# Kernel optimization log

Hardware: AMD Instinct MI355X
Metric: run time of the kernel (lower is better)

Reference implementation:

```python
import jax, jax.numpy as jnp
import numpy as np

M = 2          # interp_dim
D = 4          # interp_degree
MESH_LOWER = np.array([0.0, 0.0], dtype=np.float32)
MESH_UPPER = np.array([1.0, 1.0], dtype=np.float32)
MESH_SIZE = np.array([64, 64], dtype=np.int32)   # coe grid = mesh_size*D+1 = [257, 257]


def _lagrange_basis(t):
    """t: [N, M] local coordinate in [0, D]; returns bases [N, M, D+1].
    L_j(t) = prod_{k != j} (t - k) / (j - k)."""
    ks = jnp.arange(D + 1, dtype=t.dtype)
    tk = t[..., None] - ks                       # [N, M, D+1]
    bs = []
    for j in range(D + 1):                       # small fixed loop over D+1=5 bases
        num = jnp.ones(t.shape, t.dtype)
        denom = 1.0
        for k in range(D + 1):
            if k != j:
                num = num * tk[..., k]
                denom *= float(j - k)
        bs.append(num / denom)
    return jnp.stack(bs, axis=-1)                # [N, M, D+1]


def setup_inputs() -> dict:
    key = jax.random.key(0)
    k1, k2 = jax.random.split(key)
    inputs = jax.random.uniform(k1, (2048, 2048, M), dtype=jnp.float32)  # points in [0,1)^2
    grid = tuple(int(s) * D + 1 for s in MESH_SIZE)                      # (257, 257)
    interp_coe = jax.random.normal(k2, grid, dtype=jnp.float32)
    return {"inputs": inputs, "interp_coe": interp_coe}


def reference(inputs, interp_coe):
    size = inputs.shape
    x = inputs.reshape(-1, M)                                   # [N, M]
    lower = jnp.asarray(MESH_LOWER, x.dtype)
    upper = jnp.asarray(MESH_UPPER, x.dtype)
    msize = jnp.asarray(MESH_SIZE.astype(np.float32), x.dtype)
    u = (x - lower) / (upper - lower) * msize                   # grid coordinates
    cell = jnp.clip(jnp.floor(u), 0.0, msize - 1.0)             # [N, M] element index
    t = (u - cell) * D                                          # local coord in [0, D]
    basis = _lagrange_basis(t)                                  # [N, M, D+1]
    base = cell.astype(jnp.int32) * D                           # [N, M] global node base index
    offs = jnp.arange(D + 1, dtype=jnp.int32)
    i0 = base[:, 0, None] + offs                                # [N, D+1]
    i1 = base[:, 1, None] + offs                                # [N, D+1]
    coe = interp_coe[i0[:, :, None], i1[:, None, :]]            # [N, D+1, D+1] gathered cell coes
    out = jnp.einsum('nij,ni,nj->n', coe, basis[:, 0], basis[:, 1])
    return out.reshape(size[:-1])
```

## Files before the change

kernel.cpp:

```cpp
#include <hip/hip_runtime.h>

#define NGRID 257
#define LDS_PITCH 260
#define LDS_BYTES (LDS_PITCH * NGRID * 2)
#define BLOCK 1024
#define GRID 256
#define ITERS 16

typedef _Float16 half2_t __attribute__((ext_vector_type(2)));
typedef _Float16 half4_t __attribute__((ext_vector_type(4)));

struct __attribute__((packed, aligned(4))) f4u { float x, y, z, w; };

__device__ __forceinline__ half2_t pack2(float a, float b) {
    return __builtin_bit_cast(half2_t, __builtin_amdgcn_cvt_pkrtz(a, b));
}

__device__ __forceinline__ void lag_basis(float t, float b[5]) {
    float f0 = t;
    float f1 = t - 1.0f;
    float f2 = t - 2.0f;
    float f3 = t - 3.0f;
    float f4 = t - 4.0f;
    float p01 = f0 * f1;
    float p12 = f1 * f2;
    float p23 = f2 * f3;
    float p34 = f3 * f4;
    b[0] = p12 * p34 * (1.0f / 24.0f);
    b[1] = f0 * f2 * p34 * (-1.0f / 6.0f);
    b[2] = p01 * p34 * (1.0f / 4.0f);
    b[3] = p01 * f2 * f4 * (-1.0f / 6.0f);
    b[4] = p01 * p23 * (1.0f / 24.0f);
}

__device__ __forceinline__ float eval_pt(const _Float16* __restrict__ lds,
                                         float x0, float x1) {
    float u0 = x0 * 64.0f, u1 = x1 * 64.0f;
    int ic0 = (int)u0;
    int ic1 = (int)u1;
    float t0 = __builtin_amdgcn_fractf(u0) * 4.0f;
    float t1 = __builtin_amdgcn_fractf(u1) * 4.0f;

    const _Float16* base  = lds + (ic0 * 4) * LDS_PITCH + ic1 * 4;
    const _Float16* base2 = base + 2 * LDS_PITCH;

    half4_t lo0 = *(const half4_t*)(base);
    half4_t lo1 = *(const half4_t*)(base + LDS_PITCH);
    half4_t lo2 = *(const half4_t*)(base2);
    half4_t lo3 = *(const half4_t*)(base2 + LDS_PITCH);
    half4_t lo4 = *(const half4_t*)(base2 + 2 * LDS_PITCH);
    half2_t h0 = *(const half2_t*)(base + 4);
    half2_t h1 = *(const half2_t*)(base + LDS_PITCH + 4);
    half2_t h2 = *(const half2_t*)(base2 + 4);
    half2_t h3 = *(const half2_t*)(base2 + LDS_PITCH + 4);
    half2_t h4 = *(const half2_t*)(base2 + 2 * LDS_PITCH + 4);

    float b0[5], b1[5];
    lag_basis(t0, b0);
    lag_basis(t1, b1);
    half2_t b01 = pack2(b1[0], b1[1]);
    half2_t b23 = pack2(b1[2], b1[3]);

    half4_t lo[5] = { lo0, lo1, lo2, lo3, lo4 };
    half2_t hi[5] = { h0, h1, h2, h3, h4 };
    float rd[5];
#pragma unroll
    for (int i = 0; i < 5; ++i) {
        half2_t xy = __builtin_shufflevector(lo[i], lo[i], 0, 1);
        half2_t zw = __builtin_shufflevector(lo[i], lo[i], 2, 3);
        float r = (float)hi[i][0] * b1[4];
        r = __builtin_amdgcn_fdot2(zw, b23, r, false);
        r = __builtin_amdgcn_fdot2(xy, b01, r, false);
        rd[i] = r;
    }
    float accA = b0[4] * rd[4];
    accA = fmaf(b0[0], rd[0], accA);
    accA = fmaf(b0[2], rd[2], accA);
    float accB = b0[1] * rd[1];
    accB = fmaf(b0[3], rd[3], accB);
    return accA + accB;
}

__launch_bounds__(BLOCK, 4)
__global__ void lagrange_kernel(const float* __restrict__ inputs,
                                const float* __restrict__ coe,
                                float* __restrict__ out,
                                int npts) {
    extern __shared__ _Float16 lds[];
    const int t = threadIdx.x;

#pragma unroll
    for (int k = 0; k < 16; ++k) {
        int g = t + k * BLOCK;
        int r = g >> 6;
        int c4 = (g & 63) << 2;
        f4u q = *(const f4u*)(coe + r * NGRID + c4);
        half4_t h = { (_Float16)q.x, (_Float16)q.y,
                      (_Float16)q.z, (_Float16)q.w };
        *(half4_t*)(lds + r * LDS_PITCH + c4) = h;
    }
    if (t < 64) {
        int c4 = t << 2;
        f4u q = *(const f4u*)(coe + 256 * NGRID + c4);
        half4_t h = { (_Float16)q.x, (_Float16)q.y,
                      (_Float16)q.z, (_Float16)q.w };
        *(half4_t*)(lds + 256 * LDS_PITCH + c4) = h;
    }
    if (t < NGRID) {
        lds[t * LDS_PITCH + 256] = (_Float16)coe[t * NGRID + 256];
    }
    __syncthreads();

    const float2* __restrict__ in2 = (const float2*)inputs;
    const int tid = blockIdx.x * BLOCK + t;
    const int stride = GRID * BLOCK;
    (void)npts;

    float2 w0 = in2[tid];
    float2 w1 = in2[tid + stride];
#pragma unroll
    for (int k = 0; k < ITERS; ++k) {
        float2 w2;
        if (k + 2 < ITERS) w2 = in2[tid + (k + 2) * stride];
        float r = eval_pt(lds, w0.x, w0.y);
        __builtin_nontemporal_store(r, &out[tid + k * stride]);
        w0 = w1;
        w1 = w2;
    }
}

extern "C" void kernel_launch(void* const* d_in, const int* in_sizes, int n_in,
                              void* d_out, int out_size, void* d_ws, size_t ws_size,
                              hipStream_t stream) {
    const float* inputs = (const float*)d_in[0];
    const float* coe    = (const float*)d_in[1];
    float* out = (float*)d_out;
    int npts = out_size;

    (void)hipFuncSetAttribute((const void*)lagrange_kernel,
                              hipFuncAttributeMaxDynamicSharedMemorySize,
                              LDS_BYTES);

    dim3 grid(GRID), block(BLOCK);
    hipLaunchKernelGGL(lagrange_kernel, grid, block, LDS_BYTES, stream,
                       inputs, coe, out, npts);
}
```

Before: 84.87 us.

## Repack coefficient LDS into row-pair interleaved layout with swizzled tail table

```diff
diff --git a/kernel.cpp b/kernel.cpp
--- a/kernel.cpp
+++ b/kernel.cpp
@@ -1,15 +1,18 @@
 #include <hip/hip_runtime.h>
 
-#define NGRID 257
-#define LDS_PITCH 260
-#define LDS_BYTES (LDS_PITCH * NGRID * 2)
 #define BLOCK 1024
 #define GRID 256
 #define ITERS 16
 
+#define MAIN_HALFS (128 * 512)
+#define T_OFF_H    MAIN_HALFS
+#define LDS_BYTES  (131072 + 32768)
+
 typedef _Float16 half2_t __attribute__((ext_vector_type(2)));
 typedef _Float16 half4_t __attribute__((ext_vector_type(4)));
+typedef _Float16 half8_t __attribute__((ext_vector_type(8)));
 
+struct __attribute__((packed, aligned(4))) f2u { float x, y; };
 struct __attribute__((packed, aligned(4))) f4u { float x, y, z, w; };
 
 __device__ __forceinline__ half2_t pack2(float a, float b) {
@@ -34,50 +37,63 @@
 }
 
 __device__ __forceinline__ float eval_pt(const _Float16* __restrict__ lds,
+                                         const float* __restrict__ grow256,
                                          float x0, float x1) {
     float u0 = x0 * 64.0f, u1 = x1 * 64.0f;
-    int ic0 = (int)u0;
-    int ic1 = (int)u1;
+    int i0 = (int)u0;
+    int i1 = (int)u1;
     float t0 = __builtin_amdgcn_fractf(u0) * 4.0f;
     float t1 = __builtin_amdgcn_fractf(u1) * 4.0f;
 
-    const _Float16* base  = lds + (ic0 * 4) * LDS_PITCH + ic1 * 4;
-    const _Float16* base2 = base + 2 * LDS_PITCH;
+    const _Float16* mbase = lds + i0 * 1024 + i1 * 8;
+    half8_t m0 = *(const half8_t*)(mbase);
+    half8_t m1 = *(const half8_t*)(mbase + 512);
+    const _Float16* mb3 = mbase + ((i0 < 63) ? 1024 : 512);
+    half8_t m2 = *(const half8_t*)(mb3);
 
-    half4_t lo0 = *(const half4_t*)(base);
-    half4_t lo1 = *(const half4_t*)(base + LDS_PITCH);
-    half4_t lo2 = *(const half4_t*)(base2);
-    half4_t lo3 = *(const half4_t*)(base2 + LDS_PITCH);
-    half4_t lo4 = *(const half4_t*)(base2 + 2 * LDS_PITCH);
-    half2_t h0 = *(const half2_t*)(base + 4);
-    half2_t h1 = *(const half2_t*)(base + LDS_PITCH + 4);
-    half2_t h2 = *(const half2_t*)(base2 + 4);
-    half2_t h3 = *(const half2_t*)(base2 + LDS_PITCH + 4);
-    half2_t h4 = *(const half2_t*)(base2 + 2 * LDS_PITCH + 4);
+    const _Float16* tb = lds + T_OFF_H + i1 * 256;
+    int s  = (i0 + i1) & 63;
+    half4_t tv = *(const half4_t*)(tb + s * 4);
+    int i0c = (i0 < 63) ? i0 : 62;
+    int s2 = (i0c + 1 + i1) & 63;
+    half2_t tw = *(const half2_t*)(tb + s2 * 4);
+
+    const float* g = grow256 + i1 * 4;
+    f4u g4 = *(const f4u*)g;
+    float gc = g[4];
 
     float b0[5], b1[5];
     lag_basis(t0, b0);
     lag_basis(t1, b1);
-    half2_t b01 = pack2(b1[0], b1[1]);
-    half2_t b23 = pack2(b1[2], b1[3]);
+    half2_t q01 = pack2(b0[0], b0[1]);
+    half2_t q23 = pack2(b0[2], b0[3]);
+    float w4m = (i0 < 63) ? b0[4] : 0.0f;
+    float w63 = b0[4] - w4m;
+    half2_t q4m = pack2(w4m, 0.0f);
 
-    half4_t lo[5] = { lo0, lo1, lo2, lo3, lo4 };
-    half2_t hi[5] = { h0, h1, h2, h3, h4 };
-    float rd[5];
-#pragma unroll
-    for (int i = 0; i < 5; ++i) {
-        half2_t xy = __builtin_shufflevector(lo[i], lo[i], 0, 1);
-        half2_t zw = __builtin_shufflevector(lo[i], lo[i], 2, 3);
-        float r = (float)hi[i][0] * b1[4];
-        r = __builtin_amdgcn_fdot2(zw, b23, r, false);
-        r = __builtin_amdgcn_fdot2(xy, b01, r, false);
-        rd[i] = r;
-    }
-    float accA = b0[4] * rd[4];
-    accA = fmaf(b0[0], rd[0], accA);
-    accA = fmaf(b0[2], rd[2], accA);
-    float accB = b0[1] * rd[1];
-    accB = fmaf(b0[3], rd[3], accB);
+#define DWP(v, d) __builtin_shufflevector((v), (v), 2*(d), 2*(d)+1)
+    float cd0 = __builtin_amdgcn_fdot2(DWP(m0,0), q01,
+                __builtin_amdgcn_fdot2(DWP(m1,0), q23,
+                __builtin_amdgcn_fdot2(DWP(m2,0), q4m, fmaf(w63, g4.x, 0.0f), false), false), false);
+    float cd1 = __builtin_amdgcn_fdot2(DWP(m0,1), q01,
+                __builtin_amdgcn_fdot2(DWP(m1,1), q23,
+                __builtin_amdgcn_fdot2(DWP(m2,1), q4m, fmaf(w63, g4.y, 0.0f), false), false), false);
+    float cd2 = __builtin_amdgcn_fdot2(DWP(m0,2), q01,
+                __builtin_amdgcn_fdot2(DWP(m1,2), q23,
+                __builtin_amdgcn_fdot2(DWP(m2,2), q4m, fmaf(w63, g4.z, 0.0f), false), false), false);
+    float cd3 = __builtin_amdgcn_fdot2(DWP(m0,3), q01,
+                __builtin_amdgcn_fdot2(DWP(m1,3), q23,
+                __builtin_amdgcn_fdot2(DWP(m2,3), q4m, fmaf(w63, g4.w, 0.0f), false), false), false);
+    float cd4 = __builtin_amdgcn_fdot2(__builtin_shufflevector(tv, tv, 0, 1), q01,
+                __builtin_amdgcn_fdot2(__builtin_shufflevector(tv, tv, 2, 3), q23,
+                __builtin_amdgcn_fdot2(tw, q4m, fmaf(w63, gc, 0.0f), false), false), false);
+#undef DWP
+
+    float accA = cd0 * b1[0];
+    accA = fmaf(cd2, b1[2], accA);
+    accA = fmaf(cd4, b1[4], accA);
+    float accB = cd1 * b1[1];
+    accB = fmaf(cd3, b1[3], accB);
     return accA + accB;
 }
 
@@ -91,27 +107,32 @@
 
 #pragma unroll
     for (int k = 0; k < 16; ++k) {
-        int g = t + k * BLOCK;
-        int r = g >> 6;
-        int c4 = (g & 63) << 2;
-        f4u q = *(const f4u*)(coe + r * NGRID + c4);
-        half4_t h = { (_Float16)q.x, (_Float16)q.y,
-                      (_Float16)q.z, (_Float16)q.w };
-        *(half4_t*)(lds + r * LDS_PITCH + c4) = h;
+        int T = t + k * BLOCK;
+        int p  = T >> 7;
+        int cd = T & 127;
+        const float* src = coe + (2 * p) * 257 + 2 * cd;
+        f2u A = *(const f2u*)(src);
+        f2u B = *(const f2u*)(src + 257);
+        half4_t h = { (_Float16)A.x, (_Float16)B.x,
+                      (_Float16)A.y, (_Float16)B.y };
+        *(half4_t*)(lds + p * 512 + cd * 4) = h;
     }
-    if (t < 64) {
-        int c4 = t << 2;
-        f4u q = *(const f4u*)(coe + 256 * NGRID + c4);
-        half4_t h = { (_Float16)q.x, (_Float16)q.y,
-                      (_Float16)q.z, (_Float16)q.w };
-        *(half4_t*)(lds + 256 * LDS_PITCH + c4) = h;
-    }
-    if (t < NGRID) {
-        lds[t * LDS_PITCH + 256] = (_Float16)coe[t * NGRID + 256];
+#pragma unroll
+    for (int j = 0; j < 8; ++j) {
+        int T = t + j * BLOCK;
+        int kp = T & 63;
+        int hp = T >> 6;
+        const float* src = coe + (2 * hp) * 257 + 4 * kp + 4;
+        float a = src[0];
+        float b = src[257];
+        half2_t h2 = { (_Float16)a, (_Float16)b };
+        int pos = (2 * hp + 4 * kp) & 255;
+        *(half2_t*)(lds + T_OFF_H + kp * 256 + pos) = h2;
     }
     __syncthreads();
 
     const float2* __restrict__ in2 = (const float2*)inputs;
+    const float* __restrict__ grow256 = coe + 256 * 257;
     const int tid = blockIdx.x * BLOCK + t;
     const int stride = GRID * BLOCK;
     (void)npts;
@@ -122,7 +143,7 @@
     for (int k = 0; k < ITERS; ++k) {
         float2 w2;
         if (k + 2 < ITERS) w2 = in2[tid + (k + 2) * stride];
-        float r = eval_pt(lds, w0.x, w0.y);
+        float r = eval_pt(lds, grow256, w0.x, w0.y);
         __builtin_nontemporal_store(r, &out[tid + k * stride]);
         w0 = w1;
         w1 = w2;
```

Result: slower. 90.46 us (+6.6%).
